# Kernel optimization log

Hardware: AMD Instinct MI355X
Metric: run time of the kernel (lower is better)

## Reference

```python
import jax, jax.numpy as jnp
import numpy as np

R_EARTH_KM = 6371.0

def haversine(lat1, lon1, lat2, lon2):
    # inputs in degrees, output distance in km
    lat1, lon1, lat2, lon2 = (jnp.radians(x) for x in (lat1, lon1, lat2, lon2))
    dlat = lat2 - lat1
    dlon = lon2 - lon1
    a = jnp.sin(dlat * 0.5) ** 2 + jnp.cos(lat1) * jnp.cos(lat2) * jnp.sin(dlon * 0.5) ** 2
    return 2.0 * R_EARTH_KM * jnp.arcsin(jnp.sqrt(jnp.clip(a, 0.0, 1.0)))

def _latlon(key, n):
    k1, k2 = jax.random.split(key)
    lat = jax.random.uniform(k1, (n,), minval=-90.0, maxval=90.0)
    lon = jax.random.uniform(k2, (n,), minval=-180.0, maxval=180.0)
    return jnp.stack([lat, lon], axis=1).astype(jnp.float32)

def setup_inputs() -> dict:
    key = jax.random.key(0)
    ks = jax.random.split(key, 12)
    B, D = 4096, 1792
    NC, NM, NF = 3000, 7000, 13000
    scale = 0.02
    return {
        'features': jax.random.normal(ks[0], (B, D), dtype=jnp.float32),
        'labels_2d': _latlon(ks[1], B),
        'coarse_partition': _latlon(ks[2], NC),
        'middle_partition': _latlon(ks[3], NM),
        'fine_partition': _latlon(ks[4], NF),
        'middle_parents': jax.random.randint(ks[5], (NM,), 0, NC, dtype=jnp.int32),
        'fine_parents': jax.random.randint(ks[6], (NF,), 0, NM, dtype=jnp.int32),
        'coarse_w': jax.random.normal(ks[7], (D, NC), dtype=jnp.float32) * scale,
        'coarse_b': jnp.zeros((NC,), dtype=jnp.float32),
        'middle_w': jax.random.normal(ks[8], (D, NM), dtype=jnp.float32) * scale,
        'middle_b': jnp.zeros((NM,), dtype=jnp.float32),
        'fine_w': jax.random.normal(ks[9], (D, NF), dtype=jnp.float32) * scale,
        'fine_b': jnp.zeros((NF,), dtype=jnp.float32),
    }

def _single_loss(labels_2d, logits, partition):
    # cartesian-product haversine cdist: [B, M]
    dists = haversine(labels_2d[:, 0:1], labels_2d[:, 1:2],
                      partition[None, :, 0], partition[None, :, 1])
    labels_index = jnp.argmin(dists, axis=1)
    logp = jax.nn.log_softmax(logits, axis=1)
    nll = -jnp.take_along_axis(logp, labels_index[:, None], axis=1)[:, 0]
    return jnp.mean(nll)

def reference(features, labels_2d, coarse_partition, middle_partition, fine_partition,
              middle_parents, fine_parents, coarse_w, coarse_b, middle_w, middle_b,
              fine_w, fine_b):
    coarse_logits = features @ coarse_w + coarse_b
    middle_logits = features @ middle_w + middle_b
    fine_logits = features @ fine_w + fine_b

    loss = (_single_loss(labels_2d, coarse_logits, coarse_partition)
            + _single_loss(labels_2d, middle_logits, middle_partition)
            + _single_loss(labels_2d, fine_logits, fine_partition))

    fine_probs = jax.nn.softmax(fine_logits, axis=1)
    middle_probs = jax.nn.softmax(middle_logits, axis=1)
    coarse_probs = jax.nn.softmax(coarse_logits, axis=1)
    # hierarchy combine: gather parent probs and multiply
    final_probs = (fine_probs
                   * middle_probs[:, fine_parents]
                   * coarse_probs[:, middle_parents[fine_parents]])

    predictions = fine_partition[jnp.argmax(final_probs, axis=1)]  # [B, 2]
    d = haversine(labels_2d[:, 0], labels_2d[:, 1], predictions[:, 0], predictions[:, 1])
    thresholds = jnp.array([1.0, 25.0, 200.0, 750.0, 2500.0], dtype=jnp.float32)
    acc = jnp.mean((d[None, :] <= thresholds[:, None]).astype(jnp.float32), axis=1)
    return loss, acc
```

## Files before the change

kernel.cpp:

```cpp
#include <hip/hip_runtime.h>
#include <hip/hip_fp16.h>
#include <math.h>

#define B_   4096
#define D_   1792
#define NC_  3000
#define NM_  7000
#define NF_  13000
#define NCP  3072
#define NMP  7168
#define NFP  13312
#define NTOT (NCP + NMP + NFP)
#define OFFC 0
#define OFFM NCP
#define OFFF (NCP + NMP)
#define FHALF 6656
#define WCHUNK 7168
#define NIT 14
#define DEG2RAD 0.017453292519943295f

typedef _Float16 half8  __attribute__((ext_vector_type(8)));
typedef _Float16 half4v __attribute__((ext_vector_type(4)));
typedef float    f32x4  __attribute__((ext_vector_type(4)));

__device__ __forceinline__ void async16(const void* g, void* l) {
  __builtin_amdgcn_global_load_lds(
      (const __attribute__((address_space(1))) void*)g,
      (__attribute__((address_space(3))) void*)l, 16, 0, 0);
}

__global__ void prep_kernel(const float* __restrict__ labels,
                            const float* __restrict__ cp, const float* __restrict__ mp,
                            const float* __restrict__ fp,
                            const float* __restrict__ cb, const float* __restrict__ mb,
                            const float* __restrict__ fb,
                            float* __restrict__ bias, float4* __restrict__ ptrig,
                            float4* __restrict__ ltrig, float* __restrict__ accum) {
  int i = blockIdx.x * 256 + threadIdx.x;
  if (i < NTOT) {
    float v = 0.f;
    if (i < OFFM)      { if (i < NC_) v = cb[i]; }
    else if (i < OFFF) { int j = i - OFFM; if (j < NM_) v = mb[j]; }
    else               { int j = i - OFFF; if (j < NF_) v = fb[j]; }
    bias[i] = v;
  }
  if (i < NC_ + NM_ + NF_) {
    const float* src; int j = i;
    if (i < NC_)            { src = cp; }
    else if (i < NC_ + NM_) { src = mp; j = i - NC_; }
    else                    { src = fp; j = i - NC_ - NM_; }
    float la = src[2 * j] * DEG2RAD, lo = src[2 * j + 1] * DEG2RAD;
    float sla, cla, slo, clo;
    sincosf(la, &sla, &cla); sincosf(lo, &slo, &clo);
    ptrig[i] = make_float4(sla, cla, slo, clo);
  }
  if (i < B_) {
    float la = labels[2 * i] * DEG2RAD, lo = labels[2 * i + 1] * DEG2RAD;
    float sla, cla, slo, clo;
    sincosf(la, &sla, &cla); sincosf(lo, &slo, &clo);
    ltrig[i] = make_float4(sla, cla, slo, clo);
  }
  if (i < 64) accum[i] = 0.f;
}

__global__ void cvt_feat(const float4* __restrict__ in, half4v* __restrict__ out) {
  int i = blockIdx.x * 256 + threadIdx.x;
  float4 v = in[i];
  half4v h;
  h[0] = (_Float16)v.x; h[1] = (_Float16)v.y; h[2] = (_Float16)v.z; h[3] = (_Float16)v.w;
  out[i] = h;
}

__global__ void transpose_w(const float* __restrict__ w, _Float16* __restrict__ wt,
                            int Nfull, int c0, int ntrue_chunk) {
  __shared__ float tile[32][33];
  int n0 = blockIdx.x * 32, k0 = blockIdx.y * 32;
  int tx = threadIdx.x, ty = threadIdx.y;
#pragma unroll
  for (int i = 0; i < 4; ++i) {
    int kk = ty + i * 8;
    int n = n0 + tx;
    float v = (n < ntrue_chunk) ? w[(size_t)(k0 + kk) * Nfull + c0 + n] : 0.f;
    tile[kk][tx] = v;
  }
  __syncthreads();
#pragma unroll
  for (int i = 0; i < 4; ++i) {
    int nn = ty + i * 8;
    wt[(size_t)(n0 + nn) * D_ + k0 + tx] = (_Float16)tile[tx][nn];
  }
}

__global__ void argmin_kernel(const float4* __restrict__ ptrig, const float4* __restrict__ ltrig,
                              int* __restrict__ lidx) {
  __shared__ float rv[256];
  __shared__ int ri[256];
  int b = blockIdx.x, tid = threadIdx.x;
  float4 lt = ltrig[b];
  const int base[3] = {0, NC_, NC_ + NM_};
  const int cnt[3]  = {NC_, NM_, NF_};
#pragma unroll
  for (int h = 0; h < 3; ++h) {
    float best = 1e30f; int bi = 0;
    for (int i = tid; i < cnt[h]; i += 256) {
      float4 pt = ptrig[base[h] + i];
      float cdla = lt.y * pt.y + lt.x * pt.x;
      float cdlo = lt.w * pt.w + lt.z * pt.z;
      float a = 0.5f * (1.f - cdla) + (lt.y * pt.y) * 0.5f * (1.f - cdlo);
      if (a < best) { best = a; bi = i; }
    }
    rv[tid] = best; ri[tid] = bi;
    __syncthreads();
    for (int o = 128; o; o >>= 1) {
      if (tid < o) {
        if (rv[tid + o] < rv[tid] || (rv[tid + o] == rv[tid] && ri[tid + o] < ri[tid])) {
          rv[tid] = rv[tid + o]; ri[tid] = ri[tid + o];
        }
      }
      __syncthreads();
    }
    if (tid == 0) lidx[h * B_ + b] = ri[0];
    __syncthreads();
  }
}

#define LOADA(abase) { _Pragma("unroll") for (int tm = 0; tm < 8; ++tm) \
    af[tm] = *(const half8*)(lds + (abase) + amB + tm * 512 + xsl); }
#define LOADBALL(bbase) { _Pragma("unroll") for (int tn = 0; tn < 4; ++tn) \
    bf[tn] = *(const half8*)(lds + (bbase) + bnB + tn * 512 + xsl); }
#define DO_MFMA32 { \
    __builtin_amdgcn_s_setprio(1); \
    _Pragma("unroll") for (int tm = 0; tm < 8; ++tm) { \
      _Pragma("unroll") for (int tn = 0; tn < 4; ++tn) \
        acc[tm][tn] = __builtin_amdgcn_mfma_f32_16x16x32_f16(af[tm], bf[tn], acc[tm][tn], 0,0,0); \
    } \
    __builtin_amdgcn_s_setprio(0); }

__global__ __launch_bounds__(512, 2) void gemm_f16(const _Float16* __restrict__ A,
                                                   const _Float16* __restrict__ Bt,
                                                   const float* __restrict__ bias,
                                                   _Float16* __restrict__ C, int coff) {
  __shared__ _Float16 lds[65536];
  const int tid = threadIdx.x;
  const int lane = tid & 63, w = tid >> 6;
  const int wm = w & 1, wn = w >> 1;
  const int q = lane >> 4, l15 = lane & 15;
  const int nwg = gridDim.x, q8 = nwg >> 3;
  const int bxr = blockIdx.x;
  const int bx = (bxr & 7) * q8 + (bxr >> 3);
  const int mt = bx & 15, nt = bx >> 4;
  const int m0 = mt * 256;
  const int nl0 = nt * 256;
  const int gn0 = coff + nl0;

  f32x4 acc[8][4];
#pragma unroll
  for (int a = 0; a < 8; ++a)
#pragma unroll
    for (int b2 = 0; b2 < 4; ++b2) acc[a][b2] = (f32x4){0.f, 0.f, 0.f, 0.f};

  const int amB = (wm * 128 + l15) * 32;
  const int bnB = (wn * 64 + l15) * 32;
  const int xsl = ((q ^ ((l15 >> 1) & 3)) << 3);
  const int kbl = (lane & 3) ^ ((lane >> 3) & 3);
  const int rr = lane >> 2;

  auto stage = [&](const _Float16* __restrict__ G, int row0, int ktile, int kh, int ldsoff) {
    const int kk = ktile * 64 + (kh * 4 + kbl) * 8;
#pragma unroll
    for (int j = 0; j < 2; ++j) {
      int seg = w * 2 + j;
      async16(G + (size_t)(row0 + seg * 16 + rr) * D_ + kk,
              (void*)(lds + ldsoff + seg * 512));
    }
  };

  half8 af[8], bf[4];

  stage(A,  m0,  0, 0, 0);
  stage(Bt, nl0, 0, 0, 32768);
  stage(A,  m0,  0, 1, 8192);
  stage(Bt, nl0, 0, 1, 40960);
  stage(A,  m0,  1, 0, 16384);
  stage(Bt, nl0, 1, 0, 49152);
  asm volatile("s_waitcnt vmcnt(4)" ::: "memory");
  __builtin_amdgcn_sched_barrier(0);
  __builtin_amdgcn_s_barrier();

#pragma unroll 1
  for (int i = 0; i < NIT; ++i) {
    const int t1 = 2 * i + 1, t2 = 2 * i + 2, t3 = 2 * i + 3;
    const bool more = (i < NIT - 1);
    LOADA(0);
    LOADBALL(32768);
    stage(A,  m0,  t1, 1, 24576);
    stage(Bt, nl0, t1, 1, 57344);
    __builtin_amdgcn_s_barrier();
    DO_MFMA32;
    __builtin_amdgcn_s_barrier();
    LOADA(8192);
    LOADBALL(40960);
    if (more) {
      stage(A,  m0,  t2, 0, 0);
      stage(Bt, nl0, t2, 0, 32768);
      asm volatile("s_waitcnt vmcnt(4)" ::: "memory");
    } else {
      asm volatile("s_waitcnt vmcnt(0)" ::: "memory");
    }
    __builtin_amdgcn_sched_barrier(0);
    __builtin_amdgcn_s_barrier();
    DO_MFMA32;
    __builtin_amdgcn_s_barrier();
    LOADA(16384);
    LOADBALL(49152);
    if (more) {
      stage(A,  m0,  t2, 1, 8192);
      stage(Bt, nl0, t2, 1, 40960);
    }
    __builtin_amdgcn_s_barrier();
    DO_MFMA32;
    __builtin_amdgcn_s_barrier();
    LOADA(24576);
    LOADBALL(57344);
    if (more) {
      stage(A,  m0,  t3, 0, 16384);
      stage(Bt, nl0, t3, 0, 49152);
      asm volatile("s_waitcnt vmcnt(4)" ::: "memory");
      __builtin_amdgcn_sched_barrier(0);
    }
    __builtin_amdgcn_s_barrier();
    DO_MFMA32;
    __builtin_amdgcn_s_barrier();
  }

  float bn[4];
#pragma unroll
  for (int tn = 0; tn < 4; ++tn) bn[tn] = bias[gn0 + wn * 64 + tn * 16 + l15];
#pragma unroll
  for (int tm = 0; tm < 8; ++tm) {
    int gm = m0 + wm * 128 + tm * 16 + q * 4;
#pragma unroll
    for (int tn = 0; tn < 4; ++tn) {
      int gn = gn0 + wn * 64 + tn * 16 + l15;
      _Float16* dst = C + (size_t)gm * NTOT + gn;
#pragma unroll
      for (int r = 0; r < 4; ++r) dst[(size_t)r * NTOT] = (_Float16)(acc[tm][tn][r] + bn[tn]);
    }
  }
}

__device__ __forceinline__ float block_lse(float m, float s, float* ms, float* ss, int tid) {
  ms[tid] = m; ss[tid] = s;
  __syncthreads();
  for (int o = 128; o; o >>= 1) {
    if (tid < o) {
      float m2 = ms[tid + o], s2 = ss[tid + o];
      if (m2 > ms[tid]) { ss[tid] = s2 + ss[tid] * __expf(ms[tid] - m2); ms[tid] = m2; }
      else ss[tid] += s2 * __expf(m2 - ms[tid]);
    }
    __syncthreads();
  }
  float r = ms[0] + logf(ss[0]);
  __syncthreads();
  return r;
}

__global__ __launch_bounds__(256) void final_kernel(const _Float16* __restrict__ logits,
                                                    const int* __restrict__ mpar,
                                                    const int* __restrict__ fpar,
                                                    const float4* __restrict__ ptrig,
                                                    const float4* __restrict__ ltrig,
                                                    const int* __restrict__ lidx,
                                                    float* __restrict__ nll_buf,
                                                    float* __restrict__ accum) {
  __shared__ float co[NC_];
  __shared__ float par[NM_];
  __shared__ float ms[256], ss[256];
  __shared__ int ri[256];
  int b = blockIdx.x, tid = threadIdx.x;
  const _Float16* row = logits + (size_t)b * NTOT;

  float m = -1e30f, s = 0.f;
  {
    const half8* rc = (const half8*)(row + OFFC);
    for (int i = tid; i < NC_ / 8; i += 256) {
      half8 v = rc[i];
      float x[8];
#pragma unroll
      for (int j = 0; j < 8; ++j) x[j] = (float)v[j];
      float vm = fmaxf(fmaxf(fmaxf(x[0], x[1]), fmaxf(x[2], x[3])),
                       fmaxf(fmaxf(x[4], x[5]), fmaxf(x[6], x[7])));
      if (vm > m) { s *= __expf(m - vm); m = vm; }
#pragma unroll
      for (int j = 0; j < 8; ++j) s += __expf(x[j] - m);
      f32x4 lo = {x[0], x[1], x[2], x[3]}, hi = {x[4], x[5], x[6], x[7]};
      *(f32x4*)(co + i * 8)     = lo;
      *(f32x4*)(co + i * 8 + 4) = hi;
    }
  }
  float lseC = block_lse(m, s, ms, ss, tid);

  m = -1e30f; s = 0.f;
  {
    const half8* rm = (const half8*)(row + OFFM);
    const int4* mp4 = (const int4*)mpar;
    for (int i = tid; i < NM_ / 8; i += 256) {
      half8 v = rm[i];
      int4 p0 = mp4[2 * i], p1 = mp4[2 * i + 1];
      float x[8];
#pragma unroll
      for (int j = 0; j < 8; ++j) x[j] = (float)v[j];
      float vm = fmaxf(fmaxf(fmaxf(x[0], x[1]), fmaxf(x[2], x[3])),
                       fmaxf(fmaxf(x[4], x[5]), fmaxf(x[6], x[7])));
      if (vm > m) { s *= __expf(m - vm); m = vm; }
#pragma unroll
      for (int j = 0; j < 8; ++j) s += __expf(x[j] - m);
      int pj[8] = {p0.x, p0.y, p0.z, p0.w, p1.x, p1.y, p1.z, p1.w};
      f32x4 lo = {x[0] + co[pj[0]], x[1] + co[pj[1]], x[2] + co[pj[2]], x[3] + co[pj[3]]};
      f32x4 hi = {x[4] + co[pj[4]], x[5] + co[pj[5]], x[6] + co[pj[6]], x[7] + co[pj[7]]};
      *(f32x4*)(par + i * 8)     = lo;
      *(f32x4*)(par + i * 8 + 4) = hi;
    }
  }
  float lseM = block_lse(m, s, ms, ss, tid);

  m = -1e30f; s = 0.f;
  float best = -1e30f; int bi = 0;
  {
    const half8* rf = (const half8*)(row + OFFF);
    const int4* fp4 = (const int4*)fpar;
    for (int i = tid; i < NF_ / 8; i += 256) {
      half8 v = rf[i];
      int4 p0 = fp4[2 * i], p1 = fp4[2 * i + 1];
      float x[8];
#pragma unroll
      for (int j = 0; j < 8; ++j) x[j] = (float)v[j];
      float vm = fmaxf(fmaxf(fmaxf(x[0], x[1]), fmaxf(x[2], x[3])),
                       fmaxf(fmaxf(x[4], x[5]), fmaxf(x[6], x[7])));
      if (vm > m) { s *= __expf(m - vm); m = vm; }
#pragma unroll
      for (int j = 0; j < 8; ++j) s += __expf(x[j] - m);
      int pj[8] = {p0.x, p0.y, p0.z, p0.w, p1.x, p1.y, p1.z, p1.w};
#pragma unroll
      for (int j = 0; j < 8; ++j) {
        float vv = x[j] + par[pj[j]];
        if (vv > best) { best = vv; bi = i * 8 + j; }
      }
    }
  }
  float lseF = block_lse(m, s, ms, ss, tid);

  ms[tid] = best; ri[tid] = bi;
  __syncthreads();
  for (int o = 128; o; o >>= 1) {
    if (tid < o) {
      if (ms[tid + o] > ms[tid] || (ms[tid + o] == ms[tid] && ri[tid + o] < ri[tid])) {
        ms[tid] = ms[tid + o]; ri[tid] = ri[tid + o];
      }
    }
    __syncthreads();
  }

  if (tid == 0) {
    int ic = lidx[b], im = lidx[B_ + b], ifn = lidx[2 * B_ + b];
    nll_buf[b] = (lseC - (float)row[OFFC + ic])
               + (lseM - (float)row[OFFM + im])
               + (lseF - (float)row[OFFF + ifn]);
    float4 pt = ptrig[NC_ + NM_ + ri[0]];
    float4 lt = ltrig[b];
    float cdla = lt.y * pt.y + lt.x * pt.x;
    float cdlo = lt.w * pt.w + lt.z * pt.z;
    float a = 0.5f * (1.f - cdla) + (lt.y * pt.y) * 0.5f * (1.f - cdlo);
    a = fminf(fmaxf(a, 0.f), 1.f);
    float d = 2.f * 6371.f * asinf(sqrtf(a));
    const float thr[5] = {1.f, 25.f, 200.f, 750.f, 2500.f};
#pragma unroll
    for (int j = 0; j < 5; ++j)
      if (d <= thr[j]) atomicAdd(accum + 1 + j, 1.f);
  }
}

__global__ void finish_kernel(const float* __restrict__ accum,
                              const float* __restrict__ nll, float* __restrict__ out) {
  __shared__ float sh[256];
  int tid = threadIdx.x;
  float s = 0.f;
  for (int i = tid; i < B_; i += 256) s += nll[i];
  sh[tid] = s;
  __syncthreads();
  for (int o = 128; o; o >>= 1) { if (tid < o) sh[tid] += sh[tid + o]; __syncthreads(); }
  if (tid == 0) out[0] = sh[0] * (1.f / 4096.f);
  if (tid >= 1 && tid < 6) out[tid] = accum[tid] * (1.f / 4096.f);
}

extern "C" void kernel_launch(void* const* d_in, const int* in_sizes, int n_in,
                              void* d_out, int out_size, void* d_ws, size_t ws_size,
                              hipStream_t stream) {
  (void)in_sizes; (void)n_in; (void)out_size; (void)ws_size;
  const float* features = (const float*)d_in[0];
  const float* labels   = (const float*)d_in[1];
  const float* cpart    = (const float*)d_in[2];
  const float* mpart    = (const float*)d_in[3];
  const float* fpart    = (const float*)d_in[4];
  const int*   mpar     = (const int*)d_in[5];
  const int*   fpar     = (const int*)d_in[6];
  const float* cw       = (const float*)d_in[7];
  const float* cb       = (const float*)d_in[8];
  const float* mw       = (const float*)d_in[9];
  const float* mb       = (const float*)d_in[10];
  const float* fw       = (const float*)d_in[11];
  const float* fb       = (const float*)d_in[12];
  float* out = (float*)d_out;

  char* ws = (char*)d_ws;
  size_t off = 0;
  auto alloc = [&](size_t bytes) {
    char* p = ws + off;
    off += (bytes + 255) & ~(size_t)255;
    return p;
  };
  _Float16* feat16 = (_Float16*)alloc((size_t)B_ * D_ * 2);
  _Float16* wTbuf  = (_Float16*)alloc((size_t)WCHUNK * D_ * 2);
  _Float16* logits = (_Float16*)alloc((size_t)B_ * NTOT * 2);
  float*    bias   = (float*)alloc((size_t)NTOT * 4);
  float4*   ptrig  = (float4*)alloc((size_t)(NC_ + NM_ + NF_) * 16);
  float4*   ltrig  = (float4*)alloc((size_t)B_ * 16);
  int*      lidx   = (int*)alloc((size_t)3 * B_ * 4);
  float*    nll    = (float*)alloc((size_t)B_ * 4);
  float*    accum  = (float*)alloc(64 * 4);

  prep_kernel<<<dim3(NTOT / 256), dim3(256), 0, stream>>>(labels, cpart, mpart, fpart,
                                                          cb, mb, fb, bias, ptrig, ltrig, accum);
  cvt_feat<<<dim3(B_ * D_ / 4 / 256), dim3(256), 0, stream>>>((const float4*)features,
                                                              (half4v*)feat16);
  argmin_kernel<<<dim3(B_), dim3(256), 0, stream>>>(ptrig, ltrig, lidx);

  transpose_w<<<dim3(NCP / 32, D_ / 32), dim3(32, 8), 0, stream>>>(cw, wTbuf, NC_, 0, NC_);
  gemm_f16<<<dim3(16 * (NCP / 256)), dim3(512), 0, stream>>>(feat16, wTbuf, bias, logits, OFFC);

  transpose_w<<<dim3(NMP / 32, D_ / 32), dim3(32, 8), 0, stream>>>(mw, wTbuf, NM_, 0, NM_);
  gemm_f16<<<dim3(16 * (NMP / 256)), dim3(512), 0, stream>>>(feat16, wTbuf, bias, logits, OFFM);

  transpose_w<<<dim3(FHALF / 32, D_ / 32), dim3(32, 8), 0, stream>>>(fw, wTbuf, NF_, 0, FHALF);
  gemm_f16<<<dim3(16 * (FHALF / 256)), dim3(512), 0, stream>>>(feat16, wTbuf, bias, logits, OFFF);

  transpose_w<<<dim3(FHALF / 32, D_ / 32), dim3(32, 8), 0, stream>>>(fw, wTbuf, NF_, FHALF, NF_ - FHALF);
  gemm_f16<<<dim3(16 * (FHALF / 256)), dim3(512), 0, stream>>>(feat16, wTbuf, bias, logits, OFFF + FHALF);

  final_kernel<<<dim3(B_), dim3(256), 0, stream>>>(logits, mpar, fpar, ptrig, ltrig,
                                                   lidx, nll, accum);
  finish_kernel<<<dim3(1), dim3(256), 0, stream>>>(accum, nll, out);
}
```

Baseline: 800.5 us.

## Rebalance GEMM launches into three equal chunks and deepen LDS pipeline

```diff
diff --git a/kernel.cpp b/kernel.cpp
--- a/kernel.cpp
+++ b/kernel.cpp
@@ -14,9 +14,7 @@
 #define OFFC 0
 #define OFFM NCP
 #define OFFF (NCP + NMP)
-#define FHALF 6656
-#define WCHUNK 7168
-#define NIT 14
+#define WROWS 8192
 #define DEG2RAD 0.017453292519943295f
 
 typedef _Float16 half8  __attribute__((ext_vector_type(8)));
@@ -124,18 +122,6 @@
   }
 }
 
-#define LOADA(abase) { _Pragma("unroll") for (int tm = 0; tm < 8; ++tm) \
-    af[tm] = *(const half8*)(lds + (abase) + amB + tm * 512 + xsl); }
-#define LOADBALL(bbase) { _Pragma("unroll") for (int tn = 0; tn < 4; ++tn) \
-    bf[tn] = *(const half8*)(lds + (bbase) + bnB + tn * 512 + xsl); }
-#define DO_MFMA32 { \
-    __builtin_amdgcn_s_setprio(1); \
-    _Pragma("unroll") for (int tm = 0; tm < 8; ++tm) { \
-      _Pragma("unroll") for (int tn = 0; tn < 4; ++tn) \
-        acc[tm][tn] = __builtin_amdgcn_mfma_f32_16x16x32_f16(af[tm], bf[tn], acc[tm][tn], 0,0,0); \
-    } \
-    __builtin_amdgcn_s_setprio(0); }
-
 __global__ __launch_bounds__(512, 2) void gemm_f16(const _Float16* __restrict__ A,
                                                    const _Float16* __restrict__ Bt,
                                                    const float* __restrict__ bias,
@@ -145,7 +131,7 @@
   const int lane = tid & 63, w = tid >> 6;
   const int wm = w & 1, wn = w >> 1;
   const int q = lane >> 4, l15 = lane & 15;
-  const int nwg = gridDim.x, q8 = nwg >> 3;
+  const int q8 = gridDim.x >> 3;
   const int bxr = blockIdx.x;
   const int bx = (bxr & 7) * q8 + (bxr >> 3);
   const int mt = bx & 15, nt = bx >> 4;
@@ -165,73 +151,83 @@
   const int kbl = (lane & 3) ^ ((lane >> 3) & 3);
   const int rr = lane >> 2;
 
-  auto stage = [&](const _Float16* __restrict__ G, int row0, int ktile, int kh, int ldsoff) {
-    const int kk = ktile * 64 + (kh * 4 + kbl) * 8;
+  auto stageP = [&](int r, int P) {
+    const int kk = P * 32 + kbl * 8;
 #pragma unroll
     for (int j = 0; j < 2; ++j) {
       int seg = w * 2 + j;
-      async16(G + (size_t)(row0 + seg * 16 + rr) * D_ + kk,
-              (void*)(lds + ldsoff + seg * 512));
+      async16(A  + (size_t)(m0  + seg * 16 + rr) * D_ + kk,
+              (void*)(lds + r * 8192 + seg * 512));
+      async16(Bt + (size_t)(nl0 + seg * 16 + rr) * D_ + kk,
+              (void*)(lds + 32768 + r * 8192 + seg * 512));
     }
   };
 
   half8 af[8], bf[4];
 
-  stage(A,  m0,  0, 0, 0);
-  stage(Bt, nl0, 0, 0, 32768);
-  stage(A,  m0,  0, 1, 8192);
-  stage(Bt, nl0, 0, 1, 40960);
-  stage(A,  m0,  1, 0, 16384);
-  stage(Bt, nl0, 1, 0, 49152);
-  asm volatile("s_waitcnt vmcnt(4)" ::: "memory");
+#define PHASE(RS, RN, WAITSTR, DOSTAGE, PST) { \
+    if (DOSTAGE) stageP(RS, PST); \
+    __builtin_amdgcn_s_setprio(1); \
+    _Pragma("unroll") for (int tm = 0; tm < 8; ++tm) { \
+      _Pragma("unroll") for (int tn = 0; tn < 4; ++tn) \
+        acc[tm][tn] = __builtin_amdgcn_mfma_f32_16x16x32_f16(af[tm], bf[tn], acc[tm][tn], 0, 0, 0); \
+      af[tm] = *(const half8*)(lds + (RN) * 8192 + amB + tm * 512 + xsl); \
+    } \
+    __builtin_amdgcn_s_setprio(0); \
+    _Pragma("unroll") for (int tn = 0; tn < 4; ++tn) \
+      bf[tn] = *(const half8*)(lds + 32768 + (RN) * 8192 + bnB + tn * 512 + xsl); \
+    asm volatile(WAITSTR ::: "memory"); \
+    __builtin_amdgcn_sched_barrier(0); \
+    __builtin_amdgcn_s_barrier(); }
+
+  stageP(0, 0); stageP(1, 1); stageP(2, 2); stageP(3, 3);
+  asm volatile("s_waitcnt vmcnt(8)" ::: "memory");
   __builtin_amdgcn_sched_barrier(0);
   __builtin_amdgcn_s_barrier();
+#pragma unroll
+  for (int tm = 0; tm < 8; ++tm)
+    af[tm] = *(const half8*)(lds + amB + tm * 512 + xsl);
+#pragma unroll
+  for (int tn = 0; tn < 4; ++tn)
+    bf[tn] = *(const half8*)(lds + 32768 + bnB + tn * 512 + xsl);
+  asm volatile("s_waitcnt lgkmcnt(0)" ::: "memory");
+  __builtin_amdgcn_sched_barrier(0);
+  __builtin_amdgcn_s_barrier();
 
 #pragma unroll 1
-  for (int i = 0; i < NIT; ++i) {
-    const int t1 = 2 * i + 1, t2 = 2 * i + 2, t3 = 2 * i + 3;
-    const bool more = (i < NIT - 1);
-    LOADA(0);
-    LOADBALL(32768);
-    stage(A,  m0,  t1, 1, 24576);
-    stage(Bt, nl0, t1, 1, 57344);
-    __builtin_amdgcn_s_barrier();
-    DO_MFMA32;
-    __builtin_amdgcn_s_barrier();
-    LOADA(8192);
-    LOADBALL(40960);
-    if (more) {
-      stage(A,  m0,  t2, 0, 0);
-      stage(Bt, nl0, t2, 0, 32768);
-      asm volatile("s_waitcnt vmcnt(4)" ::: "memory");
-    } else {
-      asm volatile("s_waitcnt vmcnt(0)" ::: "memory");
-    }
-    __builtin_amdgcn_sched_barrier(0);
-    __builtin_amdgcn_s_barrier();
-    DO_MFMA32;
-    __builtin_amdgcn_s_barrier();
-    LOADA(16384);
-    LOADBALL(49152);
-    if (more) {
-      stage(A,  m0,  t2, 1, 8192);
-      stage(Bt, nl0, t2, 1, 40960);
-    }
-    __builtin_amdgcn_s_barrier();
-    DO_MFMA32;
-    __builtin_amdgcn_s_barrier();
-    LOADA(24576);
-    LOADBALL(57344);
-    if (more) {
-      stage(A,  m0,  t3, 0, 16384);
-      stage(Bt, nl0, t3, 0, 49152);
-      asm volatile("s_waitcnt vmcnt(4)" ::: "memory");
-      __builtin_amdgcn_sched_barrier(0);
-    }
-    __builtin_amdgcn_s_barrier();
-    DO_MFMA32;
-    __builtin_amdgcn_s_barrier();
-  }
+  for (int i = 0; i < 13; ++i) {
+    const int P0 = 4 * i;
+    PHASE(0, 1, "s_waitcnt vmcnt(8) lgkmcnt(0)", true, P0 + 4);
+    PHASE(1, 2, "s_waitcnt vmcnt(8) lgkmcnt(0)", true, P0 + 5);
+    PHASE(2, 3, "s_waitcnt vmcnt(8) lgkmcnt(0)", true, P0 + 6);
+    PHASE(3, 0, "s_waitcnt vmcnt(8) lgkmcnt(0)", true, P0 + 7);
+  }
+  PHASE(0, 1, "s_waitcnt vmcnt(4) lgkmcnt(0)", false, 0);
+  PHASE(0, 2, "s_waitcnt vmcnt(0) lgkmcnt(0)", false, 0);
+  {
+    __builtin_amdgcn_s_setprio(1);
+#pragma unroll
+    for (int tm = 0; tm < 8; ++tm) {
+#pragma unroll
+      for (int tn = 0; tn < 4; ++tn)
+        acc[tm][tn] = __builtin_amdgcn_mfma_f32_16x16x32_f16(af[tm], bf[tn], acc[tm][tn], 0, 0, 0);
+      af[tm] = *(const half8*)(lds + 3 * 8192 + amB + tm * 512 + xsl);
+    }
+    __builtin_amdgcn_s_setprio(0);
+#pragma unroll
+    for (int tn = 0; tn < 4; ++tn)
+      bf[tn] = *(const half8*)(lds + 32768 + 3 * 8192 + bnB + tn * 512 + xsl);
+  }
+  {
+    __builtin_amdgcn_s_setprio(1);
+#pragma unroll
+    for (int tm = 0; tm < 8; ++tm)
+#pragma unroll
+      for (int tn = 0; tn < 4; ++tn)
+        acc[tm][tn] = __builtin_amdgcn_mfma_f32_16x16x32_f16(af[tm], bf[tn], acc[tm][tn], 0, 0, 0);
+    __builtin_amdgcn_s_setprio(0);
+  }
+#undef PHASE
 
   float bn[4];
 #pragma unroll
@@ -420,7 +416,7 @@
     return p;
   };
   _Float16* feat16 = (_Float16*)alloc((size_t)B_ * D_ * 2);
-  _Float16* wTbuf  = (_Float16*)alloc((size_t)WCHUNK * D_ * 2);
+  _Float16* wTbuf  = (_Float16*)alloc((size_t)WROWS * D_ * 2);
   _Float16* logits = (_Float16*)alloc((size_t)B_ * NTOT * 2);
   float*    bias   = (float*)alloc((size_t)NTOT * 4);
   float4*   ptrig  = (float4*)alloc((size_t)(NC_ + NM_ + NF_) * 16);
@@ -435,17 +431,16 @@
                                                               (half4v*)feat16);
   argmin_kernel<<<dim3(B_), dim3(256), 0, stream>>>(ptrig, ltrig, lidx);
 
-  transpose_w<<<dim3(NCP / 32, D_ / 32), dim3(32, 8), 0, stream>>>(cw, wTbuf, NC_, 0, NC_);
-  gemm_f16<<<dim3(16 * (NCP / 256)), dim3(512), 0, stream>>>(feat16, wTbuf, bias, logits, OFFC);
-
-  transpose_w<<<dim3(NMP / 32, D_ / 32), dim3(32, 8), 0, stream>>>(mw, wTbuf, NM_, 0, NM_);
-  gemm_f16<<<dim3(16 * (NMP / 256)), dim3(512), 0, stream>>>(feat16, wTbuf, bias, logits, OFFM);
-
-  transpose_w<<<dim3(FHALF / 32, D_ / 32), dim3(32, 8), 0, stream>>>(fw, wTbuf, NF_, 0, FHALF);
-  gemm_f16<<<dim3(16 * (FHALF / 256)), dim3(512), 0, stream>>>(feat16, wTbuf, bias, logits, OFFF);
-
-  transpose_w<<<dim3(FHALF / 32, D_ / 32), dim3(32, 8), 0, stream>>>(fw, wTbuf, NF_, FHALF, NF_ - FHALF);
-  gemm_f16<<<dim3(16 * (FHALF / 256)), dim3(512), 0, stream>>>(feat16, wTbuf, bias, logits, OFFF + FHALF);
+  transpose_w<<<dim3(3072 / 32, D_ / 32), dim3(32, 8), 0, stream>>>(cw, wTbuf, NC_, 0, NC_);
+  transpose_w<<<dim3(5120 / 32, D_ / 32), dim3(32, 8), 0, stream>>>(mw, wTbuf + (size_t)3072 * D_, NM_, 0, 5120);
+  gemm_f16<<<dim3(512), dim3(512), 0, stream>>>(feat16, wTbuf, bias, logits, 0);
+
+  transpose_w<<<dim3(2048 / 32, D_ / 32), dim3(32, 8), 0, stream>>>(mw, wTbuf, NM_, 5120, NM_ - 5120);
+  transpose_w<<<dim3(6144 / 32, D_ / 32), dim3(32, 8), 0, stream>>>(fw, wTbuf + (size_t)2048 * D_, NF_, 0, 6144);
+  gemm_f16<<<dim3(512), dim3(512), 0, stream>>>(feat16, wTbuf, bias, logits, 8192);
+
+  transpose_w<<<dim3(7168 / 32, D_ / 32), dim3(32, 8), 0, stream>>>(fw, wTbuf, NF_, 6144, NF_ - 6144);
+  gemm_f16<<<dim3(448), dim3(512), 0, stream>>>(feat16, wTbuf, bias, logits, 16384);
 
   final_kernel<<<dim3(B_), dim3(256), 0, stream>>>(logits, mpar, fpar, ptrig, ltrig,
                                                    lidx, nll, accum);
```

Result: faster. 748.6 us (-6.5%).
